# Kernel optimization log

Measured on AMD Instinct MI355X. Metric: run time of the kernel, lower is better.

Reference implementation:

```python
import jax, jax.numpy as jnp
import numpy as np

D_MODEL = 4096
N_HEADS = 16
D_HEAD = D_MODEL // N_HEADS  # 256
ROT_DIMS = 64
SEQ = 2048
D_FF = 4 * D_MODEL


def _rotate_every_two(x):
    # x: [s, h, r]; interleave (-x2, x1)
    x1 = x[:, :, ::2]
    x2 = x[:, :, 1::2]
    return jnp.stack((-x2, x1), axis=-1).reshape(x.shape)


def _fixed_pos_embedding(seq_len, rot_dims, dtype):
    inv_freq = 1.0 / (10000.0 ** (np.arange(0, rot_dims, 2) / rot_dims))
    sinusoid = np.einsum('i,j->ij', np.arange(seq_len), inv_freq)  # [s, r/2]
    return jnp.asarray(np.sin(sinusoid), dtype), jnp.asarray(np.cos(sinusoid), dtype)


def _apply_rope(x, sin, cos):
    # x: [s, h, r]; sin/cos: [s, r/2] -> repeat each element twice -> [s, 1, r]
    sin = jnp.repeat(sin, 2, axis=-1)[:, None, :]
    cos = jnp.repeat(cos, 2, axis=-1)[:, None, :]
    return x * cos + _rotate_every_two(x) * sin


def setup_inputs() -> dict:
    key = jax.random.key(0)
    ks = jax.random.split(key, 10)
    s = lambda fan_in: 1.0 / np.sqrt(fan_in)
    return {
        'x': jax.random.normal(ks[0], (SEQ, D_MODEL), jnp.float32),
        'attn_bias': jnp.zeros((SEQ, SEQ), jnp.float32),
        'ln_scale': jnp.ones((D_MODEL,), jnp.float32),
        'ln_offset': jnp.zeros((D_MODEL,), jnp.float32),
        'wq': jax.random.normal(ks[1], (D_MODEL, D_MODEL), jnp.float32) * s(D_MODEL),
        'wk': jax.random.normal(ks[2], (D_MODEL, D_MODEL), jnp.float32) * s(D_MODEL),
        'wv': jax.random.normal(ks[3], (D_MODEL, D_MODEL), jnp.float32) * s(D_MODEL),
        'wo': jax.random.normal(ks[4], (D_MODEL, D_MODEL), jnp.float32) * s(D_MODEL),
        'w1': jax.random.normal(ks[5], (D_MODEL, D_FF), jnp.float32) * s(D_MODEL),
        'b1': jnp.zeros((D_FF,), jnp.float32),
        'w2': jax.random.normal(ks[6], (D_FF, D_MODEL), jnp.float32) * s(D_FF),
        'b2': jnp.zeros((D_MODEL,), jnp.float32),
    }


def reference(x, attn_bias, ln_scale, ln_offset, wq, wk, wv, wo, w1, b1, w2, b2):
    seq_len = x.shape[0]
    # ReplicatedLayerNorm (single shard => collectives are identity)
    mean = jnp.mean(x, axis=-1, keepdims=True)
    var = jnp.var(x, axis=-1, keepdims=True)
    xn = ln_scale * jax.lax.rsqrt(var + 1e-5) * (x - mean) + ln_offset

    # QKV projections (no bias) -> [s, h, dh]
    q = (xn @ wq).reshape(seq_len, N_HEADS, D_HEAD)
    v = (xn @ wv).reshape(seq_len, N_HEADS, D_HEAD)
    k = (xn @ wk).reshape(seq_len, N_HEADS, D_HEAD)

    # causal bias + external bias
    causal = jnp.tril(jnp.ones((seq_len, seq_len), x.dtype))
    bias = -1e10 * (1.0 - causal) + attn_bias

    # rotary on first ROT_DIMS dims of each head
    sin, cos = _fixed_pos_embedding(seq_len, ROT_DIMS, x.dtype)
    q = jnp.concatenate([_apply_rope(q[:, :, :ROT_DIMS], sin, cos), q[:, :, ROT_DIMS:]], axis=-1)
    k = jnp.concatenate([_apply_rope(k[:, :, :ROT_DIMS], sin, cos), k[:, :, ROT_DIMS:]], axis=-1)

    logits = jnp.einsum('thd,Thd->htT', q, k) / np.sqrt(D_HEAD).astype(x.dtype)
    logits = logits + bias
    weights = jax.nn.softmax(logits, axis=-1)
    attn_vec = jnp.einsum('htT,Thd->thd', weights, v).reshape(seq_len, D_MODEL)
    attn_out = attn_vec @ wo

    # FF: Linear -> gelu (approx, haiku/jax default) -> Linear
    dense_out = jax.nn.gelu(xn @ w1 + b1) @ w2 + b2

    return attn_out + dense_out
```

## Files before the change

kernel.cpp:

```cpp
#include <hip/hip_runtime.h>
#include <math.h>

typedef unsigned short u16;
typedef unsigned int   u32;
typedef __attribute__((ext_vector_type(8))) short bf16x8;
typedef __attribute__((ext_vector_type(4))) float f32x4;
typedef __attribute__((ext_vector_type(4))) u16   u16x4;
typedef __attribute__((ext_vector_type(8))) u16   u16x8;

#define MFMA(a,b,c) __builtin_amdgcn_mfma_f32_16x16x32_bf16((a),(b),(c),0,0,0)

__device__ __forceinline__ u16 f2bf(float f) {
    u32 u = __float_as_uint(f);
    u32 r = (u + 0x7fffu + ((u >> 16) & 1u)) >> 16;
    return (u16)r;
}
__device__ __forceinline__ float bf2f(u16 h) { return __uint_as_float(((u32)h) << 16); }

__global__ void sincos_kernel(float* __restrict__ st, float* __restrict__ ct) {
    int idx = blockIdx.x * 256 + threadIdx.x;
    int t = idx >> 5, j = idx & 31;
    double inv = pow(10000.0, -(double)j / 32.0);
    double a = (double)t * inv;
    st[idx] = (float)sin(a);
    ct[idx] = (float)cos(a);
}

__global__ __launch_bounds__(256) void ln_kernel(
    const float* __restrict__ x, const float* __restrict__ sc,
    const float* __restrict__ ofs, u16* __restrict__ Oh, u16* __restrict__ Ol) {
    const int row = blockIdx.x, tid = threadIdx.x;
    const float* xr = x + (size_t)row * 4096;
    float4 v[4];
    float s1 = 0.f, s2 = 0.f;
#pragma unroll
    for (int i = 0; i < 4; i++) {
        v[i] = *(const float4*)&xr[i * 1024 + tid * 4];
        s1 += v[i].x + v[i].y + v[i].z + v[i].w;
        s2 += v[i].x * v[i].x + v[i].y * v[i].y + v[i].z * v[i].z + v[i].w * v[i].w;
    }
#pragma unroll
    for (int m = 1; m < 64; m <<= 1) { s1 += __shfl_xor(s1, m); s2 += __shfl_xor(s2, m); }
    __shared__ float red[8];
    int w = tid >> 6;
    if ((tid & 63) == 0) { red[w] = s1; red[4 + w] = s2; }
    __syncthreads();
    s1 = red[0] + red[1] + red[2] + red[3];
    s2 = red[4] + red[5] + red[6] + red[7];
    float mean = s1 * (1.0f / 4096.0f);
    float var  = s2 * (1.0f / 4096.0f) - mean * mean;
    float rs   = 1.0f / sqrtf(var + 1e-5f);
#pragma unroll
    for (int i = 0; i < 4; i++) {
        int c0 = i * 1024 + tid * 4;
        float xs[4] = { v[i].x, v[i].y, v[i].z, v[i].w };
        u16x4 hv, lv;
#pragma unroll
        for (int j = 0; j < 4; j++) {
            float xn = sc[c0 + j] * rs * (xs[j] - mean) + ofs[c0 + j];
            u16 hh = f2bf(xn);
            hv[j] = hh;
            lv[j] = f2bf(xn - bf2f(hh));
        }
        *(u16x4*)&Oh[(size_t)row * 4096 + c0] = hv;
        *(u16x4*)&Ol[(size_t)row * 4096 + c0] = lv;
    }
}

__global__ __launch_bounds__(256) void rope_kernel(
    u16* __restrict__ qh, u16* __restrict__ ql, u16* __restrict__ kh, u16* __restrict__ kl,
    const float* __restrict__ st, const float* __restrict__ ct) {
    int gid = blockIdx.x * 256 + threadIdx.x;
    int t  = gid >> 9;
    int hh_ = (gid >> 5) & 15;
    int j2 = gid & 31;
    size_t base = (size_t)t * 4096 + (size_t)hh_ * 256 + (size_t)j2 * 2;
    float s = st[t * 32 + j2], c = ct[t * 32 + j2];
    {
        float x1 = bf2f(qh[base]) + bf2f(ql[base]);
        float x2 = bf2f(qh[base + 1]) + bf2f(ql[base + 1]);
        float o1 = x1 * c - x2 * s, o2 = x2 * c + x1 * s;
        u16 h1 = f2bf(o1); qh[base] = h1;     ql[base] = f2bf(o1 - bf2f(h1));
        u16 h2 = f2bf(o2); qh[base + 1] = h2; ql[base + 1] = f2bf(o2 - bf2f(h2));
    }
    {
        float x1 = bf2f(kh[base]) + bf2f(kl[base]);
        float x2 = bf2f(kh[base + 1]) + bf2f(kl[base + 1]);
        float o1 = x1 * c - x2 * s, o2 = x2 * c + x1 * s;
        u16 h1 = f2bf(o1); kh[base] = h1;     kl[base] = f2bf(o1 - bf2f(h1));
        u16 h2 = f2bf(o2); kh[base + 1] = h2; kl[base + 1] = f2bf(o2 - bf2f(h2));
    }
}

enum { EPI_F32 = 0, EPI_SPLIT = 1, EPI_GELU = 2, EPI_FINAL = 3 };

template <int EPI>
__global__ __launch_bounds__(256, 2) void gemm_kernel(
    const u16* __restrict__ Ah, const u16* __restrict__ Al,
    const float* __restrict__ B, int M, int N, int K,
    float* __restrict__ Cf, u16* __restrict__ Oh, u16* __restrict__ Ol,
    const float* __restrict__ bias, const float* __restrict__ addin) {
    __shared__ __align__(16) u16 LA[2][128 * 40];
    __shared__ __align__(16) u16 LB[2][128 * 40];
    const int tid = threadIdx.x;
    const int lane = tid & 63, w = tid >> 6;
    const int wm = (w >> 1) * 64, wn = (w & 1) * 64;
    const size_t n0 = (size_t)blockIdx.x * 128, m0 = (size_t)blockIdx.y * 128;
    const int fr = lane & 15, g = lane >> 4;
    const int ar = tid >> 2, as = tid & 3;
    const int bkg = tid >> 5, bng = tid & 31;
    f32x4 acc[4][4] = {};

    for (int k0 = 0; k0 < K; k0 += 32) {
        __syncthreads();
#pragma unroll
        for (int i = 0; i < 2; i++) {
            int row = ar + i * 64;
            size_t gs = (m0 + row) * (size_t)K + k0 + as * 8;
            *(u16x8*)&LA[0][row * 40 + as * 8] = *(const u16x8*)&Ah[gs];
            *(u16x8*)&LA[1][row * 40 + as * 8] = *(const u16x8*)&Al[gs];
        }
        float4 rv[4];
#pragma unroll
        for (int i = 0; i < 4; i++)
            rv[i] = *(const float4*)&B[(size_t)(k0 + bkg * 4 + i) * N + n0 + bng * 4];
#pragma unroll
        for (int j = 0; j < 4; j++) {
            float v0 = (&rv[0].x)[j], v1 = (&rv[1].x)[j], v2 = (&rv[2].x)[j], v3 = (&rv[3].x)[j];
            u16 h0 = f2bf(v0), h1 = f2bf(v1), h2 = f2bf(v2), h3 = f2bf(v3);
            u16x4 hv = { h0, h1, h2, h3 };
            u16x4 lv = { f2bf(v0 - bf2f(h0)), f2bf(v1 - bf2f(h1)),
                         f2bf(v2 - bf2f(h2)), f2bf(v3 - bf2f(h3)) };
            *(u16x4*)&LB[0][(bng * 4 + j) * 40 + bkg * 4] = hv;
            *(u16x4*)&LB[1][(bng * 4 + j) * 40 + bkg * 4] = lv;
        }
        __syncthreads();
        bf16x8 ah[4], al_[4], bh[4], bl[4];
#pragma unroll
        for (int m = 0; m < 4; m++) {
            ah[m]  = *(const bf16x8*)&LA[0][(wm + m * 16 + fr) * 40 + g * 8];
            al_[m] = *(const bf16x8*)&LA[1][(wm + m * 16 + fr) * 40 + g * 8];
        }
#pragma unroll
        for (int n = 0; n < 4; n++) {
            bh[n] = *(const bf16x8*)&LB[0][(wn + n * 16 + fr) * 40 + g * 8];
            bl[n] = *(const bf16x8*)&LB[1][(wn + n * 16 + fr) * 40 + g * 8];
        }
#pragma unroll
        for (int m = 0; m < 4; m++)
#pragma unroll
            for (int n = 0; n < 4; n++) {
                acc[m][n] = MFMA(ah[m], bh[n], acc[m][n]);
                acc[m][n] = MFMA(ah[m], bl[n], acc[m][n]);
                acc[m][n] = MFMA(al_[m], bh[n], acc[m][n]);
            }
    }
#pragma unroll
    for (int m = 0; m < 4; m++)
#pragma unroll
        for (int n = 0; n < 4; n++) {
            size_t col = n0 + wn + n * 16 + fr;
#pragma unroll
            for (int r = 0; r < 4; r++) {
                size_t row = m0 + wm + m * 16 + g * 4 + r;
                float v = acc[m][n][r];
                if constexpr (EPI == EPI_F32) {
                    Cf[row * N + col] = v;
                } else if constexpr (EPI == EPI_SPLIT) {
                    u16 hh = f2bf(v);
                    Oh[row * N + col] = hh;
                    Ol[row * N + col] = f2bf(v - bf2f(hh));
                } else if constexpr (EPI == EPI_GELU) {
                    v += bias[col];
                    float t  = tanhf(0.7978845608028654f * (v + 0.044715f * v * v * v));
                    float gl = 0.5f * v * (1.0f + t);
                    u16 hh = f2bf(gl);
                    Oh[row * N + col] = hh;
                    Ol[row * N + col] = f2bf(gl - bf2f(hh));
                } else {
                    v += bias[col] + addin[row * N + col];
                    Cf[row * N + col] = v;
                }
            }
        }
}

__global__ __launch_bounds__(256, 2) void attn_kernel(
    const u16* __restrict__ Qh, const u16* __restrict__ Ql,
    const u16* __restrict__ Kh, const u16* __restrict__ Kl,
    const u16* __restrict__ Vh, const u16* __restrict__ Vl,
    const float* __restrict__ bias, u16* __restrict__ Oh, u16* __restrict__ Ol) {
    __shared__ __align__(16) u16 LKh[32 * 256], LKl[32 * 256];
    __shared__ __align__(16) u16 LVh[256 * 32], LVl[256 * 32];
    __shared__ __align__(16) u16 LP[4][2][16 * 40];
    const int tid = threadIdx.x, lane = tid & 63, w = tid >> 6;
    const int h = blockIdx.y;
    const int qb = (h < 8) ? (int)blockIdx.x : 31 - (int)blockIdx.x;
    const int fr = lane & 15, g = lane >> 4;
    const int q0 = qb * 64 + w * 16;
    const size_t DM = 4096;

    bf16x8 qfh[8], qfl[8];
    {
        size_t base = (size_t)(q0 + fr) * DM + (size_t)h * 256 + g * 8;
#pragma unroll
        for (int ks = 0; ks < 8; ks++) {
            qfh[ks] = *(const bf16x8*)&Qh[base + ks * 32];
            qfl[ks] = *(const bf16x8*)&Ql[base + ks * 32];
        }
    }
    f32x4 opv[16] = {};
    float mrun[4] = { -1e30f, -1e30f, -1e30f, -1e30f };
    float lrun[4] = {};
    const int nkb = 2 * qb + 2;

    for (int kb = 0; kb < nkb; kb++) {
        const int t0 = kb * 32;
        __syncthreads();
#pragma unroll
        for (int u = 0; u < 4; u++) {
            int id = u * 256 + tid;
            int t = id >> 5, slot = id & 31;
            size_t gs = (size_t)(t0 + t) * DM + (size_t)h * 256 + slot * 8;
            int phys = slot ^ (t & 7);
            *(u16x8*)&LKh[t * 256 + phys * 8] = *(const u16x8*)&Kh[gs];
            *(u16x8*)&LKl[t * 256 + phys * 8] = *(const u16x8*)&Kl[gs];
        }
#pragma unroll
        for (int u = 0; u < 4; u++) {
            int id = u * 256 + tid;
            int ts = id >> 8, d = id & 255;
            u16 th[8], tl[8];
#pragma unroll
            for (int j = 0; j < 8; j++) {
                size_t gs = (size_t)(t0 + ts * 8 + j) * DM + (size_t)h * 256 + d;
                th[j] = Vh[gs];
                tl[j] = Vl[gs];
            }
            int phys = ts ^ ((d ^ (d >> 2)) & 3);
            u16x8 vh = { th[0], th[1], th[2], th[3], th[4], th[5], th[6], th[7] };
            u16x8 vl = { tl[0], tl[1], tl[2], tl[3], tl[4], tl[5], tl[6], tl[7] };
            *(u16x8*)&LVh[d * 32 + phys * 8] = vh;
            *(u16x8*)&LVl[d * 32 + phys * 8] = vl;
        }
        __syncthreads();
        f32x4 sac[2] = {};
#pragma unroll
        for (int ks = 0; ks < 8; ks++)
#pragma unroll
            for (int nf = 0; nf < 2; nf++) {
                int t = nf * 16 + fr;
                int phys = (ks * 4 + g) ^ (t & 7);
                bf16x8 kfh = *(const bf16x8*)&LKh[t * 256 + phys * 8];
                bf16x8 kfl = *(const bf16x8*)&LKl[t * 256 + phys * 8];
                sac[nf] = MFMA(qfh[ks], kfh, sac[nf]);
                sac[nf] = MFMA(qfh[ks], kfl, sac[nf]);
                sac[nf] = MFMA(qfl[ks], kfh, sac[nf]);
            }
        float pvv[2][4], rmax[4];
#pragma unroll
        for (int r = 0; r < 4; r++) {
            int qrow = q0 + g * 4 + r;
            int tg0 = t0 + fr, tg1 = t0 + 16 + fr;
            float s0 = sac[0][r] * 0.0625f + bias[(size_t)qrow * 2048 + tg0] + (tg0 > qrow ? -1e10f : 0.f);
            float s1 = sac[1][r] * 0.0625f + bias[(size_t)qrow * 2048 + tg1] + (tg1 > qrow ? -1e10f : 0.f);
            pvv[0][r] = s0; pvv[1][r] = s1;
            rmax[r] = fmaxf(s0, s1);
        }
#pragma unroll
        for (int m = 1; m <= 8; m <<= 1)
#pragma unroll
            for (int r = 0; r < 4; r++) rmax[r] = fmaxf(rmax[r], __shfl_xor(rmax[r], m));
        float alpha[4], psum[4];
#pragma unroll
        for (int r = 0; r < 4; r++) {
            float mnew = fmaxf(mrun[r], rmax[r]);
            alpha[r] = expf(mrun[r] - mnew);
            mrun[r] = mnew;
            pvv[0][r] = expf(pvv[0][r] - mnew);
            pvv[1][r] = expf(pvv[1][r] - mnew);
            psum[r] = pvv[0][r] + pvv[1][r];
        }
#pragma unroll
        for (int m = 1; m <= 8; m <<= 1)
#pragma unroll
            for (int r = 0; r < 4; r++) psum[r] += __shfl_xor(psum[r], m);
#pragma unroll
        for (int r = 0; r < 4; r++) lrun[r] = lrun[r] * alpha[r] + psum[r];
#pragma unroll
        for (int nf = 0; nf < 16; nf++)
#pragma unroll
            for (int r = 0; r < 4; r++) opv[nf][r] *= alpha[r];
#pragma unroll
        for (int f = 0; f < 2; f++)
#pragma unroll
            for (int r = 0; r < 4; r++) {
                u16 ph = f2bf(pvv[f][r]);
                LP[w][0][(g * 4 + r) * 40 + f * 16 + fr] = ph;
                LP[w][1][(g * 4 + r) * 40 + f * 16 + fr] = f2bf(pvv[f][r] - bf2f(ph));
            }
        asm volatile("s_waitcnt lgkmcnt(0)" ::: "memory");
        bf16x8 pah = *(const bf16x8*)&LP[w][0][fr * 40 + g * 8];
        bf16x8 pal = *(const bf16x8*)&LP[w][1][fr * 40 + g * 8];
#pragma unroll
        for (int nf = 0; nf < 16; nf++) {
            int d = nf * 16 + fr;
            int phys = g ^ ((d ^ (d >> 2)) & 3);
            bf16x8 vfh = *(const bf16x8*)&LVh[d * 32 + phys * 8];
            bf16x8 vfl = *(const bf16x8*)&LVl[d * 32 + phys * 8];
            opv[nf] = MFMA(pah, vfh, opv[nf]);
            opv[nf] = MFMA(pah, vfl, opv[nf]);
            opv[nf] = MFMA(pal, vfh, opv[nf]);
        }
    }
#pragma unroll
    for (int nf = 0; nf < 16; nf++) {
        size_t col = (size_t)h * 256 + nf * 16 + fr;
#pragma unroll
        for (int r = 0; r < 4; r++) {
            size_t row = (size_t)(q0 + g * 4 + r);
            float v = opv[nf][r] / lrun[r];
            u16 hh = f2bf(v);
            Oh[row * DM + col] = hh;
            Ol[row * DM + col] = f2bf(v - bf2f(hh));
        }
    }
}

extern "C" void kernel_launch(void* const* d_in, const int* in_sizes, int n_in,
                              void* d_out, int out_size, void* d_ws, size_t ws_size,
                              hipStream_t stream) {
    const float* x        = (const float*)d_in[0];
    const float* attnbias = (const float*)d_in[1];
    const float* ln_scale = (const float*)d_in[2];
    const float* ln_off   = (const float*)d_in[3];
    const float* wq = (const float*)d_in[4];
    const float* wk = (const float*)d_in[5];
    const float* wv = (const float*)d_in[6];
    const float* wo = (const float*)d_in[7];
    const float* w1 = (const float*)d_in[8];
    const float* b1 = (const float*)d_in[9];
    const float* w2 = (const float*)d_in[10];
    const float* b2 = (const float*)d_in[11];
    float* out = (float*)d_out;

    char* ws = (char*)d_ws;
    size_t off = 0;
    auto alloc = [&](size_t bytes) -> void* {
        void* p = ws + off;
        off += (bytes + 255) & ~(size_t)255;
        return p;
    };
    const size_t SD  = (size_t)2048 * 4096;
    const size_t SF  = (size_t)2048 * 16384;
    u16* xnh = (u16*)alloc(SD * 2); u16* xnl = (u16*)alloc(SD * 2);
    u16* qh  = (u16*)alloc(SD * 2); u16* ql  = (u16*)alloc(SD * 2);
    u16* kh  = (u16*)alloc(SD * 2); u16* kl  = (u16*)alloc(SD * 2);
    u16* vh  = (u16*)alloc(SD * 2); u16* vl  = (u16*)alloc(SD * 2);
    u16* ath = (u16*)alloc(SD * 2); u16* atl = (u16*)alloc(SD * 2);
    u16* hh  = (u16*)alloc(SF * 2); u16* hl  = (u16*)alloc(SF * 2);
    float* stab = (float*)alloc((size_t)2048 * 32 * 4);
    float* ctab = (float*)alloc((size_t)2048 * 32 * 4);
    (void)ws_size; (void)in_sizes; (void)n_in; (void)out_size;

    sincos_kernel<<<256, 256, 0, stream>>>(stab, ctab);
    ln_kernel<<<2048, 256, 0, stream>>>(x, ln_scale, ln_off, xnh, xnl);

    dim3 g44(32, 16);
    gemm_kernel<EPI_SPLIT><<<g44, 256, 0, stream>>>(xnh, xnl, wq, 2048, 4096, 4096,
                                                    nullptr, qh, ql, nullptr, nullptr);
    gemm_kernel<EPI_SPLIT><<<g44, 256, 0, stream>>>(xnh, xnl, wk, 2048, 4096, 4096,
                                                    nullptr, kh, kl, nullptr, nullptr);
    gemm_kernel<EPI_SPLIT><<<g44, 256, 0, stream>>>(xnh, xnl, wv, 2048, 4096, 4096,
                                                    nullptr, vh, vl, nullptr, nullptr);
    rope_kernel<<<4096, 256, 0, stream>>>(qh, ql, kh, kl, stab, ctab);
    attn_kernel<<<dim3(32, 16), 256, 0, stream>>>(qh, ql, kh, kl, vh, vl, attnbias, ath, atl);
    gemm_kernel<EPI_F32><<<g44, 256, 0, stream>>>(ath, atl, wo, 2048, 4096, 4096,
                                                  out, nullptr, nullptr, nullptr, nullptr);
    gemm_kernel<EPI_GELU><<<dim3(128, 16), 256, 0, stream>>>(xnh, xnl, w1, 2048, 16384, 4096,
                                                             nullptr, hh, hl, b1, nullptr);
    gemm_kernel<EPI_FINAL><<<g44, 256, 0, stream>>>(hh, hl, w2, 2048, 4096, 16384,
                                                    out, nullptr, nullptr, b2, out);
}
```

Baseline: 4.507 ms.

## Load GEMM A tiles directly to LDS and swizzle B layout

The GEMM's A-operand tiles (hi/lo bf16) are now loaded with global_load_lds, going straight from global memory to LDS without passing through registers. The LDS row stride drops from 40 to 32 elements. The B tile gets an XOR swizzle on both the write and read offsets to avoid bank conflicts without padding. Launch bounds are raised to target 4 blocks per CU. The A tile stays unswizzled at stride 32, so its fragment reads may now bank-conflict, and the higher occupancy target can force register spills.

```diff
diff --git a/kernel.cpp b/kernel.cpp
--- a/kernel.cpp
+++ b/kernel.cpp
@@ -16,6 +16,12 @@
     return (u16)r;
 }
 __device__ __forceinline__ float bf2f(u16 h) { return __uint_as_float(((u32)h) << 16); }
+
+__device__ __forceinline__ void gload_lds16(const void* g, void* l) {
+    __builtin_amdgcn_global_load_lds(
+        (const __attribute__((address_space(1))) void*)g,
+        (__attribute__((address_space(3))) void*)l, 16, 0, 0);
+}
 
 __global__ void sincos_kernel(float* __restrict__ st, float* __restrict__ ct) {
     int idx = blockIdx.x * 256 + threadIdx.x;
@@ -95,30 +101,49 @@
 enum { EPI_F32 = 0, EPI_SPLIT = 1, EPI_GELU = 2, EPI_FINAL = 3 };
 
 template <int EPI>
-__global__ __launch_bounds__(256, 2) void gemm_kernel(
+__global__ __launch_bounds__(256, 4) void gemm_kernel(
     const u16* __restrict__ Ah, const u16* __restrict__ Al,
     const float* __restrict__ B, int M, int N, int K,
     float* __restrict__ Cf, u16* __restrict__ Oh, u16* __restrict__ Ol,
     const float* __restrict__ bias, const float* __restrict__ addin) {
-    __shared__ __align__(16) u16 LA[2][128 * 40];
-    __shared__ __align__(16) u16 LB[2][128 * 40];
+    __shared__ __align__(16) u16 LA[2][128 * 32];
+    __shared__ __align__(16) u16 LB[2][128 * 32];
     const int tid = threadIdx.x;
     const int lane = tid & 63, w = tid >> 6;
     const int wm = (w >> 1) * 64, wn = (w & 1) * 64;
     const size_t n0 = (size_t)blockIdx.x * 128, m0 = (size_t)blockIdx.y * 128;
     const int fr = lane & 15, g = lane >> 4;
-    const int ar = tid >> 2, as = tid & 3;
     const int bkg = tid >> 5, bng = tid & 31;
+
+    int roffA[4], roffB[4], woffB[4];
+#pragma unroll
+    for (int m = 0; m < 4; m++)
+        roffA[m] = (wm + m * 16 + fr) * 32 + g * 8;
+    const int bslot = g ^ ((fr >> 2) & 3);
+#pragma unroll
+    for (int nf = 0; nf < 4; nf++) {
+        int n = wn + nf * 16 + fr;
+        int physS = ((n * 4 + bslot)) ^ ((nf & 1) << 2);
+        roffB[nf] = physS * 8;
+    }
+#pragma unroll
+    for (int j = 0; j < 4; j++) {
+        int n = bng * 4 + j;
+        int physS = (n * 4 + ((bkg >> 1) ^ (bng & 3))) ^ (((bng >> 2) & 1) << 2);
+        woffB[j] = physS * 8 + (bkg & 1) * 4;
+    }
+    const int arow = lane >> 2, aslot = lane & 3;
+
     f32x4 acc[4][4] = {};
 
     for (int k0 = 0; k0 < K; k0 += 32) {
         __syncthreads();
 #pragma unroll
-        for (int i = 0; i < 2; i++) {
-            int row = ar + i * 64;
-            size_t gs = (m0 + row) * (size_t)K + k0 + as * 8;
-            *(u16x8*)&LA[0][row * 40 + as * 8] = *(const u16x8*)&Ah[gs];
-            *(u16x8*)&LA[1][row * 40 + as * 8] = *(const u16x8*)&Al[gs];
+        for (int p = 0; p < 2; p++) {
+            int rbase = w * 32 + p * 16;
+            size_t gs = (m0 + rbase + arow) * (size_t)K + k0 + aslot * 8;
+            gload_lds16(&Ah[gs], &LA[0][rbase * 32]);
+            gload_lds16(&Al[gs], &LA[1][rbase * 32]);
         }
         float4 rv[4];
 #pragma unroll
@@ -131,20 +156,20 @@
             u16x4 hv = { h0, h1, h2, h3 };
             u16x4 lv = { f2bf(v0 - bf2f(h0)), f2bf(v1 - bf2f(h1)),
                          f2bf(v2 - bf2f(h2)), f2bf(v3 - bf2f(h3)) };
-            *(u16x4*)&LB[0][(bng * 4 + j) * 40 + bkg * 4] = hv;
-            *(u16x4*)&LB[1][(bng * 4 + j) * 40 + bkg * 4] = lv;
+            *(u16x4*)&LB[0][woffB[j]] = hv;
+            *(u16x4*)&LB[1][woffB[j]] = lv;
         }
         __syncthreads();
         bf16x8 ah[4], al_[4], bh[4], bl[4];
 #pragma unroll
         for (int m = 0; m < 4; m++) {
-            ah[m]  = *(const bf16x8*)&LA[0][(wm + m * 16 + fr) * 40 + g * 8];
-            al_[m] = *(const bf16x8*)&LA[1][(wm + m * 16 + fr) * 40 + g * 8];
+            ah[m]  = *(const bf16x8*)&LA[0][roffA[m]];
+            al_[m] = *(const bf16x8*)&LA[1][roffA[m]];
         }
 #pragma unroll
         for (int n = 0; n < 4; n++) {
-            bh[n] = *(const bf16x8*)&LB[0][(wn + n * 16 + fr) * 40 + g * 8];
-            bl[n] = *(const bf16x8*)&LB[1][(wn + n * 16 + fr) * 40 + g * 8];
+            bh[n] = *(const bf16x8*)&LB[0][roffB[n]];
+            bl[n] = *(const bf16x8*)&LB[1][roffB[n]];
         }
 #pragma unroll
         for (int m = 0; m < 4; m++)
```

Measured after the change: 4.102 ms. 1.1x faster.
